# Kernel optimization log

Measured on AMD Instinct MI355X. Metric: run time of the kernel, lower is better.

## Reference

```python
import jax, jax.numpy as jnp
import numpy as np

KH = KW = 3  # deformable conv kernel
PAD = 1


def _bilinear_group(img, py, px):
    """img: [Cg,H,W]; py,px: [K,H,W] float sampling coords. Zero padding outside."""
    H, W = img.shape[-2], img.shape[-1]
    y0 = jnp.floor(py).astype(jnp.int32)
    x0 = jnp.floor(px).astype(jnp.int32)
    y1, x1 = y0 + 1, x0 + 1
    wy = py - y0.astype(py.dtype)
    wx = px - x0.astype(px.dtype)

    def g(yi, xi):
        yc = jnp.clip(yi, 0, H - 1)
        xc = jnp.clip(xi, 0, W - 1)
        v = img[:, yc, xc]  # [Cg,K,H,W]
        m = ((yi >= 0) & (yi < H) & (xi >= 0) & (xi < W)).astype(img.dtype)
        return v * m[None]

    return (g(y0, x0) * ((1 - wy) * (1 - wx))[None]
            + g(y0, x1) * ((1 - wy) * wx)[None]
            + g(y1, x0) * (wy * (1 - wx))[None]
            + g(y1, x1) * (wy * wx)[None])  # [Cg,K,H,W]


def reference(x, wh_pred, w_off, b_off, w_d, b_d):
    B, C, H, W = x.shape
    G = w_off.shape[0]          # deformable groups (= n_anchors)
    Cg = C // G
    K = KH * KW
    # grouped 1x1 conv: per anchor group, 2 -> 18 channels
    wh = wh_pred.reshape(B, G, 2, H, W)
    off = jnp.einsum('bgchw,goc->bgohw', wh, w_off) + b_off.reshape(G, 2 * K)[None, :, :, None, None]
    off = off.reshape(B, G, K, 2, H, W)  # channel layout: (dy, dx) per kernel tap
    # base sampling grid: p(h,w,k) = (h - PAD + kh, w - PAD + kw), stride 1
    ky, kx = jnp.meshgrid(jnp.arange(KH), jnp.arange(KW), indexing='ij')
    by = (ky.reshape(K) - PAD).astype(x.dtype)[:, None, None] + jnp.arange(H, dtype=x.dtype)[None, :, None]
    bx = (kx.reshape(K) - PAD).astype(x.dtype)[:, None, None] + jnp.arange(W, dtype=x.dtype)[None, None, :]
    py = off[:, :, :, 0] + by[None, None]  # [B,G,K,H,W]
    px = off[:, :, :, 1] + bx[None, None]
    xg = x.reshape(B, G, Cg, H, W)
    sample = jax.vmap(jax.vmap(_bilinear_group))(xg, py, px)  # [B,G,Cg,K,H,W]
    wd = w_d.reshape(w_d.shape[0], G, Cg, K)
    out = jnp.einsum('bgckhw,ogck->bohw', sample, wd) + b_d[None, :, None, None]
    return out


def setup_inputs() -> dict:
    key = jax.random.key(0)
    k = jax.random.split(key, 5)
    B, C, H, W, G = 8, 256, 64, 64, 4
    Co = 256
    return {
        'x': jax.random.normal(k[0], (B, C, H, W), jnp.float32),
        'wh_pred': jax.random.normal(k[1], (B, 2 * G, H, W), jnp.float32),
        'w_off': jax.random.normal(k[2], (G, 18, 2), jnp.float32) * 0.01,
        'b_off': jnp.zeros((2 * 9 * G,), jnp.float32),
        'w_d': jax.random.normal(k[3], (Co, C, 3, 3), jnp.float32) * (1.0 / np.sqrt(C * 9)),
        'b_d': jnp.zeros((Co,), jnp.float32),
    }
```

## Files before the change

### kernel.cpp

```cpp
#include <hip/hip_runtime.h>

typedef __attribute__((ext_vector_type(8))) short bh8;
typedef __attribute__((ext_vector_type(16))) float f16v;
typedef __attribute__((ext_vector_type(4))) unsigned int u32x4;

#define NTHR 512

__device__ __forceinline__ unsigned int f2bf(float f) {
    unsigned int u = __builtin_bit_cast(unsigned int, f);
    u += 0x7FFFu + ((u >> 16) & 1u);
    return u >> 16;
}
__device__ __forceinline__ float bflo(unsigned int d) {
    return __builtin_bit_cast(float, d << 16);
}
__device__ __forceinline__ float bfhi(unsigned int d) {
    return __builtin_bit_cast(float, d & 0xFFFF0000u);
}

__global__ __launch_bounds__(256) void transpose_x_kernel(
    const float* __restrict__ x, unsigned short* __restrict__ xt) {
    __shared__ float tile[64 * 65];
    const int bid = blockIdx.x;
    const int cq = bid & 3;
    const int h  = (bid >> 2) & 63;
    const int b  = bid >> 8;
    const int tid = threadIdx.x;
    const int w = tid & 63, ci = tid >> 6;
    #pragma unroll
    for (int c0 = 0; c0 < 64; c0 += 4)
        tile[(c0 + ci) * 65 + w] =
            x[(((size_t)b * 256 + cq * 64 + c0 + ci) * 64 + h) * 64 + w];
    __syncthreads();
    const int c2 = tid & 63, w2q = tid >> 6;
    #pragma unroll
    for (int w0 = 0; w0 < 64; w0 += 4) {
        int ww = w0 + w2q;
        xt[(((size_t)b * 64 + h) * 64 + ww) * 256 + cq * 64 + c2] =
            (unsigned short)f2bf(tile[c2 * 65 + ww]);
    }
}

__global__ __launch_bounds__(256) void pack_w32_kernel(const float* __restrict__ w_d,
                                                       bh8* __restrict__ bp) {
    __shared__ float ldw[32 * 289];
    const int cc = blockIdx.x >> 3;
    const int nb = blockIdx.x & 7;
    const int tid = threadIdx.x;
    for (int i = tid; i < 32 * 288; i += 256) {
        int oi = i / 288, j = i - oi * 288;
        ldw[oi * 289 + j] = w_d[((size_t)(nb * 32 + oi)) * 2304 + cc * 288 + j];
    }
    __syncthreads();
    for (int u = tid; u < 18 * 64; u += 256) {
        int tt2 = u >> 6, l = u & 63;
        int col = l & 31, hi = l >> 5;
        int tap = tt2 >> 1;
        int cb  = (tt2 & 1) * 16 + hi * 8;
        bh8 v;
        #pragma unroll
        for (int e = 0; e < 8; ++e)
            v[e] = (short)f2bf(ldw[col * 289 + (cb + e) * 9 + tap]);
        bp[((size_t)(cc * 18 + tt2) * 8 + nb) * 64 + l] = v;
    }
}

struct PK { float w00, w01, w10, w11; int A00, A01, A10, A11, sb; };

__global__ __launch_bounds__(NTHR, 4) void featadapt_mfma(
    const unsigned short* __restrict__ xt,
    const float* __restrict__ wh_pred,
    const float* __restrict__ w_off,
    const float* __restrict__ b_off,
    const float* __restrict__ b_d,
    const bh8* __restrict__ bp,
    float* __restrict__ out)
{
    extern __shared__ unsigned char lds[];
    unsigned char* samp = lds;
    unsigned char* tile = lds + 36864;
    float* whs  = (float*)(lds + 58624);
    float* woff = (float*)(lds + 60672);
    float* boff = (float*)(lds + 61248);

    const int tid  = threadIdx.x;
    const int orig = blockIdx.x;
    const int bid  = (orig & 7) * 64 + (orig >> 3);
    const int h = bid & 63;
    const int b = bid >> 6;

    {
        int j = tid >> 6, p = tid & 63;
        whs[p * 8 + j] = wh_pred[(((size_t)b * 8 + j) * 64 + h) * 64 + p];
    }
    if (tid < 144) woff[tid] = w_off[tid];
    else if (tid < 216) boff[tid - 144] = b_off[tid - 144];

    const char* xtb = (const char*)xt + (size_t)b * (64 * 64 * 512);

    auto slotsrc = [&](int s) -> int {
        int cell = s >> 2, oct = s & 3;
        int row = cell / 68, col = cell - row * 68;
        int gy = min(max(h - 2 + row, 0), 63);
        int gx = min(max(col - 2, 0), 63);
        int osrc = oct ^ ((col + (col >> 2) + row) & 3);
        return (gy * 64 + gx) * 512 + osrc * 16;
    };
    const int sg0 = slotsrc(tid);
    const int sg1 = slotsrc(tid + 512);
    const int sg2 = slotsrc(tid + 1024);
    unsigned char* const ld0 = tile + tid * 16;
    unsigned char* const ld1 = tile + 8192 + tid * 16;
    unsigned char* const ld2 = tile + 16384 + tid * 16;

    const int l  = tid & 63;
    const int wv = tid >> 6;
    const int arow = l & 31, hi = l >> 5;
    const int ab0 = arow * 576 + hi * 16;
    const int ab1 = ab0 + 32 * 576;
    const int asw = (arow & 7) << 4;

    const int pkA = wv * 72 + l;
    const int pkB = wv * 72 + 64 + (l >> 2);

    auto calcpk = [&](int pk, int g, PK& S) {
        int p = pk / 9, k = pk - p * 9;
        float wh0 = whs[p * 8 + 2 * g], wh1 = whs[p * 8 + 2 * g + 1];
        int oy = 2 * k, ox = oy + 1;
        float offy = wh0 * woff[(g * 18 + oy) * 2] + wh1 * woff[(g * 18 + oy) * 2 + 1] + boff[g * 18 + oy];
        float offx = wh0 * woff[(g * 18 + ox) * 2] + wh1 * woff[(g * 18 + ox) * 2 + 1] + boff[g * 18 + ox];
        int ky = k / 3, kx = k - ky * 3;
        float py = offy + (float)(ky - 1 + h);
        float px = offx + (float)(kx - 1 + p);
        float fy = floorf(py), fx = floorf(px);
        int y0 = (int)fy, x0 = (int)fx;
        float wy = py - fy, wx = px - fx;
        float my0 = (y0 >= 0 && y0 < 64) ? 1.f : 0.f;
        float my1 = (y0 >= -1 && y0 < 63) ? 1.f : 0.f;
        float mx0 = (x0 >= 0 && x0 < 64) ? 1.f : 0.f;
        float mx1 = (x0 >= -1 && x0 < 63) ? 1.f : 0.f;
        S.w00 = (1.f - wy) * (1.f - wx) * my0 * mx0;
        S.w01 = (1.f - wy) * wx * my0 * mx1;
        S.w10 = wy * (1.f - wx) * my1 * mx0;
        S.w11 = wy * wx * my1 * mx1;
        int r0 = y0 - (h - 2), r1 = r0 + 1;
        int c0 = x0 + 2, c1 = c0 + 1;
        S.A00 = (r0 * 68 + c0) * 64 + (((c0 + (c0 >> 2) + r0) & 3) << 4);
        S.A01 = (r0 * 68 + c1) * 64 + (((c1 + (c1 >> 2) + r0) & 3) << 4);
        S.A10 = (r1 * 68 + c0) * 64 + (((c0 + (c0 >> 2) + r1) & 3) << 4);
        S.A11 = (r1 * 68 + c1) * 64 + (((c1 + (c1 >> 2) + r1) & 3) << 4);
        S.sb  = (p * 576 + k * 64) ^ ((p & 7) << 4) ^ (((k >> 1) & 3) << 4);
    };

    auto sample_oct = [&](const PK& S, int oct) {
        int ox4 = oct << 4;
        u32x4 q00 = *(const u32x4*)(tile + (S.A00 ^ ox4));
        u32x4 q01 = *(const u32x4*)(tile + (S.A01 ^ ox4));
        u32x4 q10 = *(const u32x4*)(tile + (S.A10 ^ ox4));
        u32x4 q11 = *(const u32x4*)(tile + (S.A11 ^ ox4));
        unsigned int ow[4];
        #pragma unroll
        for (int j = 0; j < 4; ++j) {
            float sx = bflo(q00[j]) * S.w00 + bflo(q01[j]) * S.w01
                     + bflo(q10[j]) * S.w10 + bflo(q11[j]) * S.w11;
            float sy = bfhi(q00[j]) * S.w00 + bfhi(q01[j]) * S.w01
                     + bfhi(q10[j]) * S.w10 + bfhi(q11[j]) * S.w11;
            ow[j] = (__builtin_bit_cast(unsigned int, sx) >> 16)
                  | (__builtin_bit_cast(unsigned int, sy) & 0xFFFF0000u);
        }
        u32x4 o4 = {ow[0], ow[1], ow[2], ow[3]};
        *(u32x4*)(samp + (S.sb ^ ox4)) = o4;
    };

    f16v acc0, acc1;
    #pragma unroll
    for (int r = 0; r < 16; ++r) { acc0[r] = 0.f; acc1[r] = 0.f; }

    {
        u32x4 g0 = *(const u32x4*)(xtb + sg0);
        u32x4 g1 = *(const u32x4*)(xtb + sg1);
        *(u32x4*)ld0 = g0;
        *(u32x4*)ld1 = g1;
        if (tid < 336) {
            u32x4 g2 = *(const u32x4*)(xtb + sg2);
            *(u32x4*)ld2 = g2;
        }
    }
    __syncthreads();

    PK s0, s1;
    for (int g = 0; g < 4; ++g) {
        calcpk(pkA, g, s0);
        if (l < 32) calcpk(pkB, g, s1);
        #pragma unroll
        for (int sub = 0; sub < 2; ++sub) {
            const int cc = g * 2 + sub;

            u32x4 g0v, g1v, g2v;
            const int nxt = (cc + 1) * 64;
            if (cc < 7) {
                g0v = *(const u32x4*)(xtb + sg0 + nxt);
                g1v = *(const u32x4*)(xtb + sg1 + nxt);
                if (tid < 336) g2v = *(const u32x4*)(xtb + sg2 + nxt);
            }

            #pragma unroll
            for (int oct = 0; oct < 4; ++oct) sample_oct(s0, oct);
            if (l < 32) sample_oct(s1, l & 3);
            __syncthreads();

            const bh8* bpc = bp + ((size_t)cc * 18 * 8 + wv) * 64 + l;
            __builtin_amdgcn_s_setprio(1);
            #pragma unroll 6
            for (int tt2 = 0; tt2 < 18; ++tt2) {
                const int kx4 = ((tt2 >> 2) & 3) << 4;
                bh8 a0 = *(const bh8*)(samp + (((ab0 + tt2 * 32) ^ asw) ^ kx4));
                bh8 a1 = *(const bh8*)(samp + (((ab1 + tt2 * 32) ^ asw) ^ kx4));
                bh8 bw = bpc[(size_t)tt2 * 512];
                acc0 = __builtin_amdgcn_mfma_f32_32x32x16_bf16(a0, bw, acc0, 0, 0, 0);
                acc1 = __builtin_amdgcn_mfma_f32_32x32x16_bf16(a1, bw, acc1, 0, 0, 0);
            }
            __builtin_amdgcn_s_setprio(0);

            if (cc < 7) {
                *(u32x4*)ld0 = g0v;
                *(u32x4*)ld1 = g1v;
                if (tid < 336) *(u32x4*)ld2 = g2v;
            }
            __syncthreads();
        }
    }

    const int o = wv * 32 + arow;
    const float bd = b_d[o];
    const size_t ob = (((size_t)b * 256 + o) * 64 + h) * 64;
    #pragma unroll
    for (int q = 0; q < 4; ++q) {
        float4 s4a = make_float4(acc0[4 * q + 0] + bd, acc0[4 * q + 1] + bd,
                                 acc0[4 * q + 2] + bd, acc0[4 * q + 3] + bd);
        *(float4*)&out[ob + hi * 4 + q * 8] = s4a;
        float4 s4b = make_float4(acc1[4 * q + 0] + bd, acc1[4 * q + 1] + bd,
                                 acc1[4 * q + 2] + bd, acc1[4 * q + 3] + bd);
        *(float4*)&out[ob + 32 + hi * 4 + q * 8] = s4b;
    }
}

extern "C" void kernel_launch(void* const* d_in, const int* in_sizes, int n_in,
                              void* d_out, int out_size, void* d_ws, size_t ws_size,
                              hipStream_t stream) {
    const float* x     = (const float*)d_in[0];
    const float* whp   = (const float*)d_in[1];
    const float* w_off = (const float*)d_in[2];
    const float* b_off = (const float*)d_in[3];
    const float* w_d   = (const float*)d_in[4];
    const float* b_d   = (const float*)d_in[5];
    float* out = (float*)d_out;

    unsigned short* xt = (unsigned short*)d_ws;
    bh8* bp = (bh8*)((char*)d_ws + (size_t)8 * 64 * 64 * 256 * 2);

    hipLaunchKernelGGL(transpose_x_kernel, dim3(2048), dim3(256), 0, stream, x, xt);
    hipLaunchKernelGGL(pack_w32_kernel, dim3(64), dim3(256), 0, stream, w_d, bp);
    hipLaunchKernelGGL(featadapt_mfma, dim3(512), dim3(NTHR), 61536, stream,
                       xt, whp, w_off, b_off, b_d, bp, out);
}
```

Before: 85.85 us.

## Double block to 1024 threads, splitting pixel halves across extra waves

Raises the main kernel's block size from 512 to 1024 threads (16 waves). Each wave now owns one 32x32 MFMA tile (pixel half x output-channel block) instead of two. Sampling work and tile-load slots are spread across twice as many threads. The aim is more latency hiding and parallelism per block. The cost is that each B-weight fragment is loaded twice (once per pixel half), syncthreads now spans more waves, and register limits per thread become tighter.

```diff
diff --git a/kernel.cpp b/kernel.cpp
--- a/kernel.cpp
+++ b/kernel.cpp
@@ -4,7 +4,7 @@
 typedef __attribute__((ext_vector_type(16))) float f16v;
 typedef __attribute__((ext_vector_type(4))) unsigned int u32x4;
 
-#define NTHR 512
+#define NTHR 1024
 
 __device__ __forceinline__ unsigned int f2bf(float f) {
     unsigned int u = __builtin_bit_cast(unsigned int, f);
@@ -89,12 +89,14 @@
     const int h = bid & 63;
     const int b = bid >> 6;
 
-    {
+    if (tid < 512) {
         int j = tid >> 6, p = tid & 63;
         whs[p * 8 + j] = wh_pred[(((size_t)b * 8 + j) * 64 + h) * 64 + p];
-    }
-    if (tid < 144) woff[tid] = w_off[tid];
-    else if (tid < 216) boff[tid - 144] = b_off[tid - 144];
+    } else {
+        int t2 = tid - 512;
+        if (t2 < 144) woff[t2] = w_off[t2];
+        else if (t2 < 216) boff[t2 - 144] = b_off[t2 - 144];
+    }
 
     const char* xtb = (const char*)xt + (size_t)b * (64 * 64 * 512);
 
@@ -107,21 +109,22 @@
         return (gy * 64 + gx) * 512 + osrc * 16;
     };
     const int sg0 = slotsrc(tid);
-    const int sg1 = slotsrc(tid + 512);
-    const int sg2 = slotsrc(tid + 1024);
+    const int sg1 = (tid < 336) ? slotsrc(tid + 1024) : 0;
     unsigned char* const ld0 = tile + tid * 16;
-    unsigned char* const ld1 = tile + 8192 + tid * 16;
-    unsigned char* const ld2 = tile + 16384 + tid * 16;
+    unsigned char* const ld1 = tile + 16384 + tid * 16;
 
     const int l  = tid & 63;
     const int wv = tid >> 6;
+    const int im = wv >> 3;
+    const int nb = wv & 7;
     const int arow = l & 31, hi = l >> 5;
-    const int ab0 = arow * 576 + hi * 16;
-    const int ab1 = ab0 + 32 * 576;
+    const int ab  = (im * 32 + arow) * 576 + hi * 16;
     const int asw = (arow & 7) << 4;
 
-    const int pkA = wv * 72 + l;
-    const int pkB = wv * 72 + 64 + (l >> 2);
+    const int pkA = tid >> 1, ohA = tid & 1;
+    const bool hasB = ((l & 7) == 0);
+    const int eB  = wv * 8 + (l >> 3);
+    const int pkB = 512 + (eB >> 1), ohB = eB & 1;
 
     auto calcpk = [&](int pk, int g, PK& S) {
         int p = pk / 9, k = pk - p * 9;
@@ -172,18 +175,16 @@
         *(u32x4*)(samp + (S.sb ^ ox4)) = o4;
     };
 
-    f16v acc0, acc1;
-    #pragma unroll
-    for (int r = 0; r < 16; ++r) { acc0[r] = 0.f; acc1[r] = 0.f; }
+    f16v acc;
+    #pragma unroll
+    for (int r = 0; r < 16; ++r) acc[r] = 0.f;
 
     {
         u32x4 g0 = *(const u32x4*)(xtb + sg0);
-        u32x4 g1 = *(const u32x4*)(xtb + sg1);
         *(u32x4*)ld0 = g0;
-        *(u32x4*)ld1 = g1;
         if (tid < 336) {
-            u32x4 g2 = *(const u32x4*)(xtb + sg2);
-            *(u32x4*)ld2 = g2;
+            u32x4 g1 = *(const u32x4*)(xtb + sg1);
+            *(u32x4*)ld1 = g1;
         }
     }
     __syncthreads();
@@ -191,57 +192,53 @@
     PK s0, s1;
     for (int g = 0; g < 4; ++g) {
         calcpk(pkA, g, s0);
-        if (l < 32) calcpk(pkB, g, s1);
+        if (hasB) calcpk(pkB, g, s1);
         #pragma unroll
         for (int sub = 0; sub < 2; ++sub) {
             const int cc = g * 2 + sub;
 
-            u32x4 g0v, g1v, g2v;
+            u32x4 g0v, g1v;
             const int nxt = (cc + 1) * 64;
             if (cc < 7) {
                 g0v = *(const u32x4*)(xtb + sg0 + nxt);
-                g1v = *(const u32x4*)(xtb + sg1 + nxt);
-                if (tid < 336) g2v = *(const u32x4*)(xtb + sg2 + nxt);
-            }
-
-            #pragma unroll
-            for (int oct = 0; oct < 4; ++oct) sample_oct(s0, oct);
-            if (l < 32) sample_oct(s1, l & 3);
+                if (tid < 336) g1v = *(const u32x4*)(xtb + sg1 + nxt);
+            }
+
+            sample_oct(s0, ohA * 2);
+            sample_oct(s0, ohA * 2 + 1);
+            if (hasB) {
+                sample_oct(s1, ohB * 2);
+                sample_oct(s1, ohB * 2 + 1);
+            }
             __syncthreads();
 
-            const bh8* bpc = bp + ((size_t)cc * 18 * 8 + wv) * 64 + l;
+            const bh8* bpc = bp + ((size_t)cc * 18 * 8 + nb) * 64 + l;
             __builtin_amdgcn_s_setprio(1);
             #pragma unroll 6
             for (int tt2 = 0; tt2 < 18; ++tt2) {
                 const int kx4 = ((tt2 >> 2) & 3) << 4;
-                bh8 a0 = *(const bh8*)(samp + (((ab0 + tt2 * 32) ^ asw) ^ kx4));
-                bh8 a1 = *(const bh8*)(samp + (((ab1 + tt2 * 32) ^ asw) ^ kx4));
+                bh8 a = *(const bh8*)(samp + (((ab + tt2 * 32) ^ asw) ^ kx4));
                 bh8 bw = bpc[(size_t)tt2 * 512];
-                acc0 = __builtin_amdgcn_mfma_f32_32x32x16_bf16(a0, bw, acc0, 0, 0, 0);
-                acc1 = __builtin_amdgcn_mfma_f32_32x32x16_bf16(a1, bw, acc1, 0, 0, 0);
+                acc = __builtin_amdgcn_mfma_f32_32x32x16_bf16(a, bw, acc, 0, 0, 0);
             }
             __builtin_amdgcn_s_setprio(0);
 
             if (cc < 7) {
                 *(u32x4*)ld0 = g0v;
-                *(u32x4*)ld1 = g1v;
-                if (tid < 336) *(u32x4*)ld2 = g2v;
+                if (tid < 336) *(u32x4*)ld1 = g1v;
             }
             __syncthreads();
         }
     }
 
-    const int o = wv * 32 + arow;
+    const int o = nb * 32 + arow;
     const float bd = b_d[o];
-    const size_t ob = (((size_t)b * 256 + o) * 64 + h) * 64;
+    const size_t ob = (((size_t)b * 256 + o) * 64 + h) * 64 + im * 32;
     #pragma unroll
     for (int q = 0; q < 4; ++q) {
-        float4 s4a = make_float4(acc0[4 * q + 0] + bd, acc0[4 * q + 1] + bd,
-                                 acc0[4 * q + 2] + bd, acc0[4 * q + 3] + bd);
-        *(float4*)&out[ob + hi * 4 + q * 8] = s4a;
-        float4 s4b = make_float4(acc1[4 * q + 0] + bd, acc1[4 * q + 1] + bd,
-                                 acc1[4 * q + 2] + bd, acc1[4 * q + 3] + bd);
-        *(float4*)&out[ob + 32 + hi * 4 + q * 8] = s4b;
+        float4 s4 = make_float4(acc[4 * q + 0] + bd, acc[4 * q + 1] + bd,
+                                acc[4 * q + 2] + bd, acc[4 * q + 3] + bd);
+        *(float4*)&out[ob + hi * 4 + q * 8] = s4;
     }
 }
 
```

New measurement: 114.0 us. 1.33x slower.

## Halve channel chunk to 16 to shrink LDS and raise occupancy

Applied to the files above, without the earlier changes.

The channel chunk per pipeline stage drops from 32 to 16 bf16 channels, which halves the sample buffer and input tile in LDS (about 61.5KB down to 32KB) and raises the launch-bounds occupancy hint from 4 to 6. The weight packing, tile swizzle (69-wide rows, 2 octets), bilinear corner addressing and tap-to-lane mapping are reworked to match, with 16 iterations of 9 MFMA pairs instead of 8 of 18. The goal is more resident waves to hide LDS and global latency, at the cost of twice as many barriers and per-stage overheads, plus halo reloads per chunk.

```diff
diff --git a/kernel.cpp b/kernel.cpp
--- a/kernel.cpp
+++ b/kernel.cpp
@@ -41,33 +41,31 @@
     }
 }
 
-__global__ __launch_bounds__(256) void pack_w32_kernel(const float* __restrict__ w_d,
+__global__ __launch_bounds__(256) void pack_w16_kernel(const float* __restrict__ w_d,
                                                        bh8* __restrict__ bp) {
-    __shared__ float ldw[32 * 289];
+    __shared__ float ldw[32 * 145];
     const int cc = blockIdx.x >> 3;
     const int nb = blockIdx.x & 7;
     const int tid = threadIdx.x;
-    for (int i = tid; i < 32 * 288; i += 256) {
-        int oi = i / 288, j = i - oi * 288;
-        ldw[oi * 289 + j] = w_d[((size_t)(nb * 32 + oi)) * 2304 + cc * 288 + j];
+    for (int i = tid; i < 32 * 144; i += 256) {
+        int oi = i / 144, j = i - oi * 144;
+        ldw[oi * 145 + j] = w_d[(size_t)(nb * 32 + oi) * 2304 + cc * 144 + j];
     }
     __syncthreads();
-    for (int u = tid; u < 18 * 64; u += 256) {
-        int tt2 = u >> 6, l = u & 63;
-        int col = l & 31, hi = l >> 5;
-        int tap = tt2 >> 1;
-        int cb  = (tt2 & 1) * 16 + hi * 8;
+    for (int u = tid; u < 9 * 64; u += 256) {
+        int tt = u >> 6, ll = u & 63;
+        int col = ll & 31, hi2 = ll >> 5;
         bh8 v;
         #pragma unroll
         for (int e = 0; e < 8; ++e)
-            v[e] = (short)f2bf(ldw[col * 289 + (cb + e) * 9 + tap]);
-        bp[((size_t)(cc * 18 + tt2) * 8 + nb) * 64 + l] = v;
-    }
-}
-
-struct PK { float w00, w01, w10, w11; int A00, A01, A10, A11, sb; };
-
-__global__ __launch_bounds__(NTHR, 4) void featadapt_mfma(
+            v[e] = (short)f2bf(ldw[col * 145 + (hi2 * 8 + e) * 9 + tt]);
+        bp[((size_t)(cc * 9 + tt) * 8 + nb) * 64 + ll] = v;
+    }
+}
+
+struct PK { float w00, w01, w10, w11; int A00, A01, sb; };
+
+__global__ __launch_bounds__(NTHR, 6) void featadapt_mfma(
     const unsigned short* __restrict__ xt,
     const float* __restrict__ wh_pred,
     const float* __restrict__ w_off,
@@ -78,10 +76,10 @@
 {
     extern __shared__ unsigned char lds[];
     unsigned char* samp = lds;
-    unsigned char* tile = lds + 36864;
-    float* whs  = (float*)(lds + 58624);
-    float* woff = (float*)(lds + 60672);
-    float* boff = (float*)(lds + 61248);
+    unsigned char* tile = lds + 18432;
+    float* whs  = (float*)(lds + 29472);
+    float* woff = (float*)(lds + 31520);
+    float* boff = (float*)(lds + 32096);
 
     const int tid  = threadIdx.x;
     const int orig = blockIdx.x;
@@ -99,37 +97,34 @@
     const char* xtb = (const char*)xt + (size_t)b * (64 * 64 * 512);
 
     auto slotsrc = [&](int s) -> int {
-        int cell = s >> 2, oct = s & 3;
-        int row = cell / 68, col = cell - row * 68;
-        int gy = min(max(h - 2 + row, 0), 63);
-        int gx = min(max(col - 2, 0), 63);
-        int osrc = oct ^ ((col + (col >> 2) + row) & 3);
-        return (gy * 64 + gx) * 512 + osrc * 16;
+        int cell = s >> 1, j = s & 1;
+        int r = cell / 69, c = cell - r * 69;
+        int gy = min(max(h - 2 + r, 0), 63);
+        int gx = min(max(c - 2, 0), 63);
+        int od = j ^ (((c >> 2) + r) & 1);
+        return (gy * 64 + gx) * 512 + od * 16;
     };
     const int sg0 = slotsrc(tid);
-    const int sg1 = slotsrc(tid + 512);
-    const int sg2 = slotsrc(tid + 1024);
+    const int sg1 = (tid < 178) ? slotsrc(512 + tid) : 0;
     unsigned char* const ld0 = tile + tid * 16;
     unsigned char* const ld1 = tile + 8192 + tid * 16;
-    unsigned char* const ld2 = tile + 16384 + tid * 16;
 
     const int l  = tid & 63;
     const int wv = tid >> 6;
     const int arow = l & 31, hi = l >> 5;
-    const int ab0 = arow * 576 + hi * 16;
-    const int ab1 = ab0 + 32 * 576;
+    const int ab0 = arow * 288 + hi * 16;
+    const int ab1 = ab0 + 32 * 288;
     const int asw = (arow & 7) << 4;
 
-    const int pkA = wv * 72 + l;
-    const int pkB = wv * 72 + 64 + (l >> 2);
-
-    auto calcpk = [&](int pk, int g, PK& S) {
-        int p = pk / 9, k = pk - p * 9;
+    const int pM = wv * 8 + (l >> 3), tM = l & 7;
+    const int pE = wv * 8 + (l >> 1);
+
+    auto calcpk = [&](int p, int tap, int g, PK& S) {
         float wh0 = whs[p * 8 + 2 * g], wh1 = whs[p * 8 + 2 * g + 1];
-        int oy = 2 * k, ox = oy + 1;
+        int oy = 2 * tap, ox = oy + 1;
         float offy = wh0 * woff[(g * 18 + oy) * 2] + wh1 * woff[(g * 18 + oy) * 2 + 1] + boff[g * 18 + oy];
         float offx = wh0 * woff[(g * 18 + ox) * 2] + wh1 * woff[(g * 18 + ox) * 2 + 1] + boff[g * 18 + ox];
-        int ky = k / 3, kx = k - ky * 3;
+        int ky = tap / 3, kx = tap - ky * 3;
         float py = offy + (float)(ky - 1 + h);
         float px = offx + (float)(kx - 1 + p);
         float fy = floorf(py), fx = floorf(px);
@@ -143,21 +138,19 @@
         S.w01 = (1.f - wy) * wx * my0 * mx1;
         S.w10 = wy * (1.f - wx) * my1 * mx0;
         S.w11 = wy * wx * my1 * mx1;
-        int r0 = y0 - (h - 2), r1 = r0 + 1;
+        int r0 = y0 - (h - 2);
         int c0 = x0 + 2, c1 = c0 + 1;
-        S.A00 = (r0 * 68 + c0) * 64 + (((c0 + (c0 >> 2) + r0) & 3) << 4);
-        S.A01 = (r0 * 68 + c1) * 64 + (((c1 + (c1 >> 2) + r0) & 3) << 4);
-        S.A10 = (r1 * 68 + c0) * 64 + (((c0 + (c0 >> 2) + r1) & 3) << 4);
-        S.A11 = (r1 * 68 + c1) * 64 + (((c1 + (c1 >> 2) + r1) & 3) << 4);
-        S.sb  = (p * 576 + k * 64) ^ ((p & 7) << 4) ^ (((k >> 1) & 3) << 4);
+        S.A00 = (r0 * 69 + c0) * 32 + ((((c0 >> 2) + r0) & 1) << 4);
+        S.A01 = (r0 * 69 + c1) * 32 + ((((c1 >> 2) + r0) & 1) << 4);
+        S.sb  = (p * 288 + tap * 32) ^ ((p & 7) << 4);
     };
 
     auto sample_oct = [&](const PK& S, int oct) {
         int ox4 = oct << 4;
         u32x4 q00 = *(const u32x4*)(tile + (S.A00 ^ ox4));
         u32x4 q01 = *(const u32x4*)(tile + (S.A01 ^ ox4));
-        u32x4 q10 = *(const u32x4*)(tile + (S.A10 ^ ox4));
-        u32x4 q11 = *(const u32x4*)(tile + (S.A11 ^ ox4));
+        u32x4 q10 = *(const u32x4*)(tile + (((S.A00 + 2208) ^ 16) ^ ox4));
+        u32x4 q11 = *(const u32x4*)(tile + (((S.A01 + 2208) ^ 16) ^ ox4));
         unsigned int ow[4];
         #pragma unroll
         for (int j = 0; j < 4; ++j) {
@@ -177,58 +170,50 @@
     for (int r = 0; r < 16; ++r) { acc0[r] = 0.f; acc1[r] = 0.f; }
 
     {
-        u32x4 g0 = *(const u32x4*)(xtb + sg0);
-        u32x4 g1 = *(const u32x4*)(xtb + sg1);
-        *(u32x4*)ld0 = g0;
-        *(u32x4*)ld1 = g1;
-        if (tid < 336) {
-            u32x4 g2 = *(const u32x4*)(xtb + sg2);
-            *(u32x4*)ld2 = g2;
-        }
+        u32x4 t0 = *(const u32x4*)(xtb + sg0);
+        u32x4 t1;
+        if (tid < 178) t1 = *(const u32x4*)(xtb + sg1);
+        *(u32x4*)ld0 = t0;
+        if (tid < 178) *(u32x4*)ld1 = t1;
     }
     __syncthreads();
 
     PK s0, s1;
-    for (int g = 0; g < 4; ++g) {
-        calcpk(pkA, g, s0);
-        if (l < 32) calcpk(pkB, g, s1);
+    for (int cc = 0; cc < 16; ++cc) {
+        if ((cc & 3) == 0) {
+            int g = cc >> 2;
+            calcpk(pM, tM, g, s0);
+            if (l < 16) calcpk(pE, 8, g, s1);
+        }
+        u32x4 n0, n1;
+        if (cc < 15) {
+            const int off = (cc + 1) * 32;
+            n0 = *(const u32x4*)(xtb + sg0 + off);
+            if (tid < 178) n1 = *(const u32x4*)(xtb + sg1 + off);
+        }
+
+        sample_oct(s0, 0);
+        sample_oct(s0, 1);
+        if (l < 16) sample_oct(s1, l & 1);
+        __syncthreads();
+
+        const bh8* bpc = bp + ((size_t)cc * 9 * 8 + wv) * 64 + l;
+        __builtin_amdgcn_s_setprio(1);
         #pragma unroll
-        for (int sub = 0; sub < 2; ++sub) {
-            const int cc = g * 2 + sub;
-
-            u32x4 g0v, g1v, g2v;
-            const int nxt = (cc + 1) * 64;
-            if (cc < 7) {
-                g0v = *(const u32x4*)(xtb + sg0 + nxt);
-                g1v = *(const u32x4*)(xtb + sg1 + nxt);
-                if (tid < 336) g2v = *(const u32x4*)(xtb + sg2 + nxt);
-            }
-
-            #pragma unroll
-            for (int oct = 0; oct < 4; ++oct) sample_oct(s0, oct);
-            if (l < 32) sample_oct(s1, l & 3);
-            __syncthreads();
-
-            const bh8* bpc = bp + ((size_t)cc * 18 * 8 + wv) * 64 + l;
-            __builtin_amdgcn_s_setprio(1);
-            #pragma unroll 6
-            for (int tt2 = 0; tt2 < 18; ++tt2) {
-                const int kx4 = ((tt2 >> 2) & 3) << 4;
-                bh8 a0 = *(const bh8*)(samp + (((ab0 + tt2 * 32) ^ asw) ^ kx4));
-                bh8 a1 = *(const bh8*)(samp + (((ab1 + tt2 * 32) ^ asw) ^ kx4));
-                bh8 bw = bpc[(size_t)tt2 * 512];
-                acc0 = __builtin_amdgcn_mfma_f32_32x32x16_bf16(a0, bw, acc0, 0, 0, 0);
-                acc1 = __builtin_amdgcn_mfma_f32_32x32x16_bf16(a1, bw, acc1, 0, 0, 0);
-            }
-            __builtin_amdgcn_s_setprio(0);
-
-            if (cc < 7) {
-                *(u32x4*)ld0 = g0v;
-                *(u32x4*)ld1 = g1v;
-                if (tid < 336) *(u32x4*)ld2 = g2v;
-            }
-            __syncthreads();
-        }
+        for (int tt = 0; tt < 9; ++tt) {
+            bh8 a0 = *(const bh8*)(samp + ((ab0 + tt * 32) ^ asw));
+            bh8 a1 = *(const bh8*)(samp + ((ab1 + tt * 32) ^ asw));
+            bh8 bw = bpc[(size_t)tt * 512];
+            acc0 = __builtin_amdgcn_mfma_f32_32x32x16_bf16(a0, bw, acc0, 0, 0, 0);
+            acc1 = __builtin_amdgcn_mfma_f32_32x32x16_bf16(a1, bw, acc1, 0, 0, 0);
+        }
+        __builtin_amdgcn_s_setprio(0);
+
+        if (cc < 15) {
+            *(u32x4*)ld0 = n0;
+            if (tid < 178) *(u32x4*)ld1 = n1;
+        }
+        __syncthreads();
     }
 
     const int o = wv * 32 + arow;
@@ -260,7 +245,7 @@
     bh8* bp = (bh8*)((char*)d_ws + (size_t)8 * 64 * 64 * 256 * 2);
 
     hipLaunchKernelGGL(transpose_x_kernel, dim3(2048), dim3(256), 0, stream, x, xt);
-    hipLaunchKernelGGL(pack_w32_kernel, dim3(64), dim3(256), 0, stream, w_d, bp);
-    hipLaunchKernelGGL(featadapt_mfma, dim3(512), dim3(NTHR), 61536, stream,
+    hipLaunchKernelGGL(pack_w16_kernel, dim3(128), dim3(256), 0, stream, w_d, bp);
+    hipLaunchKernelGGL(featadapt_mfma, dim3(512), dim3(NTHR), 32384, stream,
                        xt, whp, w_off, b_off, b_d, bp, out);
 }
```

New measurement: 190.4 us. +121.8%, slower.
